# Optimization experiments

Measured on AMD Instinct MI355X. Metric: run time of the kernel, lower is better.

Reference implementation:

```python
import jax, jax.numpy as jnp
import numpy as np

DIM = 768
NUM_HEADS = 12
HEAD_DIM = DIM // NUM_HEADS
SCALE = HEAD_DIM ** -0.5
EPS = 1e-6


def setup_inputs() -> dict:
    key = jax.random.key(0)
    k_x, k_p, k_qkv, k_proj = jax.random.split(key, 4)
    B, N = 16, 577
    x = jax.random.normal(k_x, (B, N, DIM), dtype=jnp.float32)
    # binary keep/drop policy per token (as produced by an upstream gumbel gate)
    policy = jax.random.randint(k_p, (B, N, 1), 0, 2).astype(jnp.float32)
    Wqkv = jax.random.normal(k_qkv, (DIM, 3 * DIM), dtype=jnp.float32) * 0.02
    bqkv = jnp.zeros((3 * DIM,), dtype=jnp.float32)
    Wproj = jax.random.normal(k_proj, (DIM, DIM), dtype=jnp.float32) * 0.02
    bproj = jnp.zeros((DIM,), dtype=jnp.float32)
    return {"x": x, "policy": policy, "Wqkv": Wqkv, "bqkv": bqkv,
            "Wproj": Wproj, "bproj": bproj}


def reference(x, policy, Wqkv, bqkv, Wproj, bproj):
    B, N, C = x.shape
    # qkv projection -> [3, B, H, N, Dh]
    qkv = (x @ Wqkv + bqkv).reshape(B, N, 3, NUM_HEADS, HEAD_DIM)
    qkv = jnp.transpose(qkv, (2, 0, 3, 1, 4))
    q, k, v = qkv[0], qkv[1], qkv[2]
    # scaled attention logits [B, H, N, N]
    attn = jnp.einsum("bhnd,bhmd->bhnm", q, k) * SCALE
    # policy-masked softmax (training-mode formula: eye keeps self-attention alive)
    ap = policy.reshape(B, 1, 1, N)
    eye = jnp.eye(N, dtype=ap.dtype).reshape(1, 1, N, N)
    ap = ap + (1.0 - ap) * eye
    max_att = jnp.max(attn, axis=-1, keepdims=True)
    e = jnp.exp(attn - max_att) * ap
    attn = (e + EPS / N) / (jnp.sum(e, axis=-1, keepdims=True) + EPS)
    # attend and project
    out = jnp.einsum("bhnm,bhmd->bhnd", attn, v)
    out = jnp.transpose(out, (0, 2, 1, 3)).reshape(B, N, C)
    return out @ Wproj + bproj
```

## Files before the change

### kernel.cpp

```cpp
#include <hip/hip_runtime.h>
#include <hip/hip_bf16.h>

#define QKVC   2304
#define NHEAD  12
#define NTOK   577
#define NBATCH 16
#define NROWS  (NBATCH * NTOK)
#define NPAD   640
#define SCALE  0.125f
#define EPSV   1e-6f

typedef __bf16  bf16x8 __attribute__((ext_vector_type(8)));
typedef float   f32x4  __attribute__((ext_vector_type(4)));

__device__ __forceinline__ unsigned short f2bf(float f) {
    union { float f; unsigned u; } v; v.f = f;
    unsigned r = v.u + 0x7FFFu + ((v.u >> 16) & 1u);
    return (unsigned short)(r >> 16);
}
__device__ __forceinline__ unsigned short f2bf_trunc(float f) {
    return (unsigned short)(__float_as_uint(f) >> 16);
}
__device__ __forceinline__ f32x4 mfma16(bf16x8 a, bf16x8 b, f32x4 c) {
    return __builtin_amdgcn_mfma_f32_16x16x32_bf16(a, b, c, 0, 0, 0);
}

#define GLDS16(g, l) __builtin_amdgcn_global_load_lds( \
    (const __attribute__((address_space(1))) unsigned int*)(g), \
    (__attribute__((address_space(3))) unsigned int*)(l), 16, 0, 0)

__device__ void transpose_tile(const float* __restrict__ src, unsigned short* __restrict__ dst,
                               int K, int N, int bx, int by, int t) {
    __shared__ unsigned short lt[64 * 72];
    int n0 = bx * 64, k0 = by * 64;
    int kk = t >> 4, nn = (t & 15) * 4;
    for (int i = 0; i < 4; i++) {
        int kr = kk + i * 16;
        float4 v = *(const float4*)&src[(size_t)(k0 + kr) * N + n0 + nn];
        lt[(nn + 0) * 72 + kr] = f2bf(v.x);
        lt[(nn + 1) * 72 + kr] = f2bf(v.y);
        lt[(nn + 2) * 72 + kr] = f2bf(v.z);
        lt[(nn + 3) * 72 + kr] = f2bf(v.w);
    }
    __syncthreads();
    int n = t >> 2, seg = (t & 3) * 16;
    uint4 a = *(uint4*)&lt[n * 72 + seg];
    uint4 b = *(uint4*)&lt[n * 72 + seg + 8];
    *(uint4*)&dst[(size_t)(n0 + n) * K + k0 + seg]     = a;
    *(uint4*)&dst[(size_t)(n0 + n) * K + k0 + seg + 8] = b;
}

#define NCONV (NROWS * 768 / 4 / 256)
__global__ void k_prep(const float* __restrict__ x, unsigned short* __restrict__ xb,
                       const float* __restrict__ Wqkv, unsigned short* __restrict__ wqkvt,
                       const float* __restrict__ Wproj, unsigned short* __restrict__ wprojt) {
    int id = blockIdx.x, t = threadIdx.x;
    if (id < NCONV) {
        int idx = id * 256 + t;
        float4 v = ((const float4*)x)[idx];
        ushort4 o;
        o.x = f2bf(v.x); o.y = f2bf(v.y); o.z = f2bf(v.z); o.w = f2bf(v.w);
        ((ushort4*)xb)[idx] = o;
    } else if (id < NCONV + 432) {
        int i2 = id - NCONV;
        transpose_tile(Wqkv, wqkvt, 768, QKVC, i2 % 36, i2 / 36, t);
    } else {
        int i2 = id - NCONV - 432;
        transpose_tile(Wproj, wprojt, 768, 768, i2 % 12, i2 / 12, t);
    }
}

template <bool F32OUT>
__global__ __launch_bounds__(256, 2)
void k_gemm(const unsigned short* __restrict__ A, const unsigned short* __restrict__ B,
            const float* __restrict__ bias, void* __restrict__ outp, int Ncols,
            unsigned short* __restrict__ vt) {
    __shared__ unsigned short SL[32768];
    int t = threadIdx.x;
    int lane = t & 63, wave = t >> 6, quad = lane >> 4, l15 = lane & 15;
    int wm = wave >> 1, wn = wave & 1;
    int nT = Ncols >> 7;
    int mLocal = blockIdx.x & 7;
    int rest = blockIdx.x >> 3;
    int n0 = (rest % nT) * 128;
    int m0 = ((rest / nT) * 8 + mLocal) * 128;

    const unsigned short* ga0 = A + (size_t)(m0 + wave * 32 + (lane >> 2)) * 768 + (lane & 3) * 8;
    const unsigned short* ga1 = ga0 + (size_t)16 * 768;
    const unsigned short* gb0 = B + (size_t)(n0 + wave * 32 + (lane >> 2)) * 768 + (lane & 3) * 8;
    const unsigned short* gb1 = gb0 + (size_t)16 * 768;
    unsigned lo = wave * 1024;

    f32x4 acc[4][4] = {};

    GLDS16(ga0,      &SL[lo]);              GLDS16(ga1,      &SL[lo + 512]);
    GLDS16(ga0 + 32, &SL[4096 + lo]);       GLDS16(ga1 + 32, &SL[4096 + lo + 512]);
    GLDS16(gb0,      &SL[16384 + lo]);      GLDS16(gb1,      &SL[16384 + lo + 512]);
    GLDS16(gb0 + 32, &SL[20480 + lo]);      GLDS16(gb1 + 32, &SL[20480 + lo + 512]);

    #pragma unroll 2
    for (int kt = 0; kt < 12; kt++) {
        unsigned ab = (kt & 1) * 8192;
        unsigned bb = 16384 + ab;
        asm volatile("s_waitcnt vmcnt(0)" ::: "memory");
        asm volatile("s_barrier" ::: "memory");
        if (kt < 11) {
            unsigned na = 8192 - ab, nb = 16384 + na;
            int ko = (kt + 1) * 64;
            GLDS16(ga0 + ko,      &SL[na + lo]);        GLDS16(ga1 + ko,      &SL[na + lo + 512]);
            GLDS16(ga0 + ko + 32, &SL[na + 4096 + lo]); GLDS16(ga1 + ko + 32, &SL[na + 4096 + lo + 512]);
            GLDS16(gb0 + ko,      &SL[nb + lo]);        GLDS16(gb1 + ko,      &SL[nb + lo + 512]);
            GLDS16(gb0 + ko + 32, &SL[nb + 4096 + lo]); GLDS16(gb1 + ko + 32, &SL[nb + 4096 + lo + 512]);
        }
        for (int h = 0; h < 2; h++) {
            bf16x8 af[4], bfr[4];
            for (int i = 0; i < 4; i++) {
                af[i]  = *(const bf16x8*)&SL[ab + h * 4096 + (wm * 64 + i * 16 + l15) * 32 + quad * 8];
                bfr[i] = *(const bf16x8*)&SL[bb + h * 4096 + (wn * 64 + i * 16 + l15) * 32 + quad * 8];
            }
            for (int mi = 0; mi < 4; mi++)
                for (int ni = 0; ni < 4; ni++)
                    acc[mi][ni] = mfma16(af[mi], bfr[ni], acc[mi][ni]);
        }
    }
    asm volatile("" ::: "memory");

    if constexpr (F32OUT) {
        for (int ni = 0; ni < 4; ni++) {
            int col = n0 + wn * 64 + ni * 16 + l15;
            float bv = bias[col];
            for (int mi = 0; mi < 4; mi++) {
                int rowm = m0 + wm * 64 + mi * 16 + quad * 4;
                for (int r = 0; r < 4; r++) {
                    int m = rowm + r;
                    if (m < NROWS)
                        ((float*)outp)[(size_t)m * Ncols + col] = acc[mi][ni][r] + bv;
                }
            }
        }
    } else {
        __syncthreads();
        for (int ni = 0; ni < 4; ni++) {
            int colL = wn * 64 + ni * 16 + l15;
            float bv = bias[n0 + colL];
            for (int mi = 0; mi < 4; mi++) {
                int rowL = wm * 64 + mi * 16 + quad * 4;
                for (int r = 0; r < 4; r++)
                    SL[(rowL + r) * 132 + colL] = f2bf(acc[mi][ni][r] + bv);
            }
        }
        __syncthreads();
        if (n0 < 1536) {
            for (int rr = 0; rr < 8; rr++) {
                int row = rr * 16 + (t >> 4);
                int m = m0 + row;
                if (m < NROWS) {
                    uint4 v = *(uint4*)&SL[row * 132 + (t & 15) * 8];
                    *(uint4*)&((unsigned short*)outp)[(size_t)m * Ncols + n0 + (t & 15) * 8] = v;
                }
            }
        } else {
            int h0 = (n0 - 1536) >> 6;
            for (int i = 0; i < 32; i++) {
                int c = wave * 32 + i;
                int h = h0 + (c >> 6), d = c & 63;
                for (int half = 0; half < 2; half++) {
                    int lr = half * 64 + lane;
                    int m = m0 + lr;
                    if (m < NROWS) {
                        unsigned bbx = (unsigned)m / 577u;
                        int tok = m - (int)bbx * 577;
                        vt[(((size_t)bbx * NHEAD + h) * 64 + d) * NPAD + tok] =
                            SL[lr * 132 + c];
                    }
                }
            }
        }
    }
}

__global__ __launch_bounds__(256, 4)
void k_attn(const unsigned short* __restrict__ qkv, const unsigned short* __restrict__ vt,
            const float* __restrict__ policy, unsigned short* __restrict__ ao) {
    __shared__ unsigned short Ks[64 * 72];
    __shared__ unsigned short Vs[64 * 72];
    __shared__ unsigned short Ps[4][32 * 72];
    __shared__ float pol[NPAD];
    int t = threadIdx.x;
    int lane = t & 63, wave = t >> 6, quad = lane >> 4, l15 = lane & 15;
    int b = blockIdx.z, h = blockIdx.y, qt = blockIdx.x;
    const unsigned short* qbase = qkv + (size_t)(b * NTOK) * QKVC + h * 64;
    const unsigned short* kbase = qkv + (size_t)(b * NTOK) * QKVC + 768 + h * 64;
    const unsigned short* vbase = vt + (size_t)(b * NHEAD + h) * 64 * NPAD;

    for (int i = t; i < NPAD; i += 256)
        pol[i] = (i < NTOK) ? policy[b * NTOK + i] : 0.f;

    bf16x8 qf[2][2];
    for (int mi = 0; mi < 2; mi++) {
        const unsigned short* qp =
            qbase + (size_t)(qt * 128 + mi * 64 + wave * 16 + l15) * QKVC + quad * 8;
        qf[mi][0] = *(const bf16x8*)qp;
        qf[mi][1] = *(const bf16x8*)(qp + 32);
    }
    bf16x8 onesf;
    for (int j = 0; j < 8; j++) onesf[j] = (__bf16)1.0f;
    f32x4 o[2][4] = {};
    f32x4 ls[2] = {};
    int rowtok0[2];
    for (int mi = 0; mi < 2; mi++)
        rowtok0[mi] = qt * 128 + mi * 64 + wave * 16 + quad * 4;
    __syncthreads();

    for (int kt = 0; kt < 10; kt++) {
        int key0 = kt * 64;
        for (int i = t; i < 512; i += 256) {
            int row = i >> 3, seg = (i & 7) * 8;
            *(uint4*)&Ks[row * 72 + seg] = *(const uint4*)&kbase[(size_t)(key0 + row) * QKVC + seg];
            *(uint4*)&Vs[row * 72 + seg] = *(const uint4*)&vbase[(size_t)row * NPAD + key0 + seg];
        }
        __syncthreads();

        for (int ci = 0; ci < 4; ci++) {
            bf16x8 kf0 = *(const bf16x8*)&Ks[(ci * 16 + l15) * 72 + quad * 8];
            bf16x8 kf1 = *(const bf16x8*)&Ks[(ci * 16 + l15) * 72 + 32 + quad * 8];
            int col = key0 + ci * 16 + l15;
            float pc = pol[col];
            for (int mi = 0; mi < 2; mi++) {
                f32x4 a = {};
                a = mfma16(qf[mi][0], kf0, a);
                a = mfma16(qf[mi][1], kf1, a);
                for (int r = 0; r < 4; r++) {
                    float ap = (col == rowtok0[mi] + r) ? 1.f : pc;
                    float e = __expf(a[r] * SCALE) * ap;
                    Ps[wave][(mi * 16 + quad * 4 + r) * 72 + ci * 16 + l15] = f2bf_trunc(e);
                }
            }
        }
        __asm__ volatile("s_waitcnt lgkmcnt(0)" ::: "memory");
        bf16x8 pf[2][2];
        for (int mi = 0; mi < 2; mi++) {
            pf[mi][0] = *(const bf16x8*)&Ps[wave][(mi * 16 + l15) * 72 + quad * 8];
            pf[mi][1] = *(const bf16x8*)&Ps[wave][(mi * 16 + l15) * 72 + 32 + quad * 8];
            ls[mi] = mfma16(pf[mi][0], onesf, ls[mi]);
            ls[mi] = mfma16(pf[mi][1], onesf, ls[mi]);
        }
        for (int di = 0; di < 4; di++) {
            bf16x8 vf0 = *(const bf16x8*)&Vs[(di * 16 + l15) * 72 + quad * 8];
            bf16x8 vf1 = *(const bf16x8*)&Vs[(di * 16 + l15) * 72 + 32 + quad * 8];
            for (int mi = 0; mi < 2; mi++) {
                o[mi][di] = mfma16(pf[mi][0], vf0, o[mi][di]);
                o[mi][di] = mfma16(pf[mi][1], vf1, o[mi][di]);
            }
        }
        __syncthreads();
    }

    for (int mi = 0; mi < 2; mi++) {
        for (int r = 0; r < 4; r++) {
            int tok = rowtok0[mi] + r;
            if (tok < NTOK) {
                float inv = __builtin_amdgcn_rcpf(ls[mi][r] + EPSV);
                for (int di = 0; di < 4; di++) {
                    float val = o[mi][di][r] * inv;
                    ao[((size_t)(b * NTOK + tok)) * 768 + h * 64 + di * 16 + l15] = f2bf(val);
                }
            }
        }
    }
}

extern "C" void kernel_launch(void* const* d_in, const int* in_sizes, int n_in,
                              void* d_out, int out_size, void* d_ws, size_t ws_size,
                              hipStream_t stream) {
    const float* x      = (const float*)d_in[0];
    const float* policy = (const float*)d_in[1];
    const float* Wqkv   = (const float*)d_in[2];
    const float* bqkv   = (const float*)d_in[3];
    const float* Wproj  = (const float*)d_in[4];
    const float* bproj  = (const float*)d_in[5];
    float* out = (float*)d_out;

    unsigned short* p = (unsigned short*)d_ws;
    unsigned short* xb     = p;
    unsigned short* ao     = p; p += (size_t)NROWS * 768;
    unsigned short* wqkvt  = p; p += (size_t)QKVC * 768;
    unsigned short* wprojt = p; p += (size_t)768 * 768;
    unsigned short* qkvb   = p; p += (size_t)NROWS * QKVC;
    unsigned short* vt     = p; p += (size_t)NBATCH * NHEAD * 64 * NPAD;

    int mT = (NROWS + 127) / 128;
    int mG = (mT + 7) / 8;

    k_prep<<<NCONV + 432 + 144, 256, 0, stream>>>(x, xb, Wqkv, wqkvt, Wproj, wprojt);
    k_gemm<false><<<mG * 8 * (QKVC / 128), 256, 0, stream>>>(
        xb, wqkvt, bqkv, (void*)qkvb, QKVC, vt);
    k_attn<<<dim3(NPAD / 128, NHEAD, NBATCH), 256, 0, stream>>>(qkvb, vt, policy, ao);
    k_gemm<true><<<mG * 8 * (768 / 128), 256, 0, stream>>>(
        ao, wprojt, bproj, (void*)out, 768, nullptr);
}
```

Baseline: 203.3 us.

## Restructure GEMM to 256x128 tiles, 8 waves, 4-stage swizzled LDS pipeline

Rewrites the bf16 GEMM kernel to use 512-thread blocks computing 256x128 output tiles, with a 4-deep ring of 32-wide K slices loaded via global-to-LDS and partial vmcnt waits. It adds an XOR swizzle on LDS segments to reduce bank conflicts, s_setprio around the MFMA bursts, and an XCD-aware block remapping so that neighbouring tiles share an L2. The goal is deeper latency hiding and better operand reuse per block. In exchange it uses more LDS (96KB) and more accumulator registers per wave, and it pads the epilogue stride differently.

```diff
diff --git a/kernel.cpp b/kernel.cpp
--- a/kernel.cpp
+++ b/kernel.cpp
@@ -71,66 +71,84 @@
 }
 
 template <bool F32OUT>
-__global__ __launch_bounds__(256, 2)
+__global__ __launch_bounds__(512, 2)
 void k_gemm(const unsigned short* __restrict__ A, const unsigned short* __restrict__ B,
             const float* __restrict__ bias, void* __restrict__ outp, int Ncols,
             unsigned short* __restrict__ vt) {
-    __shared__ unsigned short SL[32768];
+    __shared__ unsigned short SL[49152];
     int t = threadIdx.x;
     int lane = t & 63, wave = t >> 6, quad = lane >> 4, l15 = lane & 15;
-    int wm = wave >> 1, wn = wave & 1;
+    int wm = wave >> 2, wn = wave & 3;
     int nT = Ncols >> 7;
-    int mLocal = blockIdx.x & 7;
-    int rest = blockIdx.x >> 3;
-    int n0 = (rest % nT) * 128;
-    int m0 = ((rest / nT) * 8 + mLocal) * 128;
-
-    const unsigned short* ga0 = A + (size_t)(m0 + wave * 32 + (lane >> 2)) * 768 + (lane & 3) * 8;
-    const unsigned short* ga1 = ga0 + (size_t)16 * 768;
-    const unsigned short* gb0 = B + (size_t)(n0 + wave * 32 + (lane >> 2)) * 768 + (lane & 3) * 8;
-    const unsigned short* gb1 = gb0 + (size_t)16 * 768;
-    unsigned lo = wave * 1024;
-
-    f32x4 acc[4][4] = {};
-
-    GLDS16(ga0,      &SL[lo]);              GLDS16(ga1,      &SL[lo + 512]);
-    GLDS16(ga0 + 32, &SL[4096 + lo]);       GLDS16(ga1 + 32, &SL[4096 + lo + 512]);
-    GLDS16(gb0,      &SL[16384 + lo]);      GLDS16(gb1,      &SL[16384 + lo + 512]);
-    GLDS16(gb0 + 32, &SL[20480 + lo]);      GLDS16(gb1 + 32, &SL[20480 + lo + 512]);
-
-    #pragma unroll 2
-    for (int kt = 0; kt < 12; kt++) {
-        unsigned ab = (kt & 1) * 8192;
-        unsigned bb = 16384 + ab;
-        asm volatile("s_waitcnt vmcnt(0)" ::: "memory");
+    int nwg = gridDim.x;
+
+    int q8 = nwg >> 3, r8 = nwg & 7;
+    int xcd = blockIdx.x & 7, idx = blockIdx.x >> 3;
+    int wg = (xcd < r8 ? xcd * (q8 + 1) : r8 * (q8 + 1) + (xcd - r8) * q8) + idx;
+    int m0 = (wg / nT) * 256;
+    int n0 = (wg % nT) * 128;
+
+    int srow = lane >> 2;
+    int sseg = (lane & 3) ^ ((lane >> 3) & 3);
+    const unsigned short* gA0 = A + (size_t)(m0 +       wave * 16 + srow) * 768 + sseg * 8;
+    const unsigned short* gA1 = A + (size_t)(m0 + 128 + wave * 16 + srow) * 768 + sseg * 8;
+    const unsigned short* gB0 = B + (size_t)(n0 +       wave * 16 + srow) * 768 + sseg * 8;
+
+    f32x4 acc[8][2] = {};
+
+    auto STAGE = [&](int sx) {
+        unsigned sa = (unsigned)(sx & 3) * 8192u + (unsigned)wave * 512u;
+        unsigned sb = 32768u + (unsigned)(sx & 3) * 4096u + (unsigned)wave * 512u;
+        int ko = sx * 32;
+        GLDS16(gA0 + ko, &SL[sa]);
+        GLDS16(gA1 + ko, &SL[sa + 4096]);
+        GLDS16(gB0 + ko, &SL[sb]);
+    };
+
+    auto STEP = [&](int s, bool stage) {
+        unsigned ab = (unsigned)(s & 3) * 8192u;
+        unsigned bb = 32768u + (unsigned)(s & 3) * 4096u;
+        unsigned ro = (unsigned)(quad ^ ((l15 >> 1) & 3)) * 8u;
+        bf16x8 af[8], bfr[2];
+        #pragma unroll
+        for (int i = 0; i < 8; i++)
+            af[i]  = *(const bf16x8*)&SL[ab + (unsigned)(wm * 128 + i * 16 + l15) * 32u + ro];
+        #pragma unroll
+        for (int i = 0; i < 2; i++)
+            bfr[i] = *(const bf16x8*)&SL[bb + (unsigned)(wn * 32 + i * 16 + l15) * 32u + ro];
+        if (stage) STAGE(s + 3);
+        asm volatile("s_waitcnt lgkmcnt(0)" ::: "memory");
+        __builtin_amdgcn_s_setprio(1);
+        #pragma unroll
+        for (int mi = 0; mi < 8; mi++)
+            #pragma unroll
+            for (int ni = 0; ni < 2; ni++)
+                acc[mi][ni] = mfma16(af[mi], bfr[ni], acc[mi][ni]);
+        __builtin_amdgcn_s_setprio(0);
+    };
+
+    STAGE(0); STAGE(1); STAGE(2);
+    for (int s = 0; s < 21; s++) {
+        asm volatile("s_waitcnt vmcnt(6)" ::: "memory");
         asm volatile("s_barrier" ::: "memory");
-        if (kt < 11) {
-            unsigned na = 8192 - ab, nb = 16384 + na;
-            int ko = (kt + 1) * 64;
-            GLDS16(ga0 + ko,      &SL[na + lo]);        GLDS16(ga1 + ko,      &SL[na + lo + 512]);
-            GLDS16(ga0 + ko + 32, &SL[na + 4096 + lo]); GLDS16(ga1 + ko + 32, &SL[na + 4096 + lo + 512]);
-            GLDS16(gb0 + ko,      &SL[nb + lo]);        GLDS16(gb1 + ko,      &SL[nb + lo + 512]);
-            GLDS16(gb0 + ko + 32, &SL[nb + 4096 + lo]); GLDS16(gb1 + ko + 32, &SL[nb + 4096 + lo + 512]);
-        }
-        for (int h = 0; h < 2; h++) {
-            bf16x8 af[4], bfr[4];
-            for (int i = 0; i < 4; i++) {
-                af[i]  = *(const bf16x8*)&SL[ab + h * 4096 + (wm * 64 + i * 16 + l15) * 32 + quad * 8];
-                bfr[i] = *(const bf16x8*)&SL[bb + h * 4096 + (wn * 64 + i * 16 + l15) * 32 + quad * 8];
-            }
-            for (int mi = 0; mi < 4; mi++)
-                for (int ni = 0; ni < 4; ni++)
-                    acc[mi][ni] = mfma16(af[mi], bfr[ni], acc[mi][ni]);
-        }
-    }
-    asm volatile("" ::: "memory");
+        STEP(s, true);
+    }
+    asm volatile("s_waitcnt vmcnt(6)" ::: "memory");
+    asm volatile("s_barrier" ::: "memory");
+    STEP(21, false);
+    asm volatile("s_waitcnt vmcnt(3)" ::: "memory");
+    asm volatile("s_barrier" ::: "memory");
+    STEP(22, false);
+    asm volatile("s_waitcnt vmcnt(0)" ::: "memory");
+    asm volatile("s_barrier" ::: "memory");
+    STEP(23, false);
 
     if constexpr (F32OUT) {
-        for (int ni = 0; ni < 4; ni++) {
-            int col = n0 + wn * 64 + ni * 16 + l15;
+        for (int ni = 0; ni < 2; ni++) {
+            int col = n0 + wn * 32 + ni * 16 + l15;
             float bv = bias[col];
-            for (int mi = 0; mi < 4; mi++) {
-                int rowm = m0 + wm * 64 + mi * 16 + quad * 4;
+            for (int mi = 0; mi < 8; mi++) {
+                int rowm = m0 + wm * 128 + mi * 16 + quad * 4;
                 for (int r = 0; r < 4; r++) {
                     int m = rowm + r;
                     if (m < NROWS)
@@ -140,38 +158,38 @@
         }
     } else {
         __syncthreads();
-        for (int ni = 0; ni < 4; ni++) {
-            int colL = wn * 64 + ni * 16 + l15;
+        for (int ni = 0; ni < 2; ni++) {
+            int colL = wn * 32 + ni * 16 + l15;
             float bv = bias[n0 + colL];
-            for (int mi = 0; mi < 4; mi++) {
-                int rowL = wm * 64 + mi * 16 + quad * 4;
+            for (int mi = 0; mi < 8; mi++) {
+                int rowL = wm * 128 + mi * 16 + quad * 4;
                 for (int r = 0; r < 4; r++)
-                    SL[(rowL + r) * 132 + colL] = f2bf(acc[mi][ni][r] + bv);
+                    SL[(rowL + r) * 136 + colL] = f2bf(acc[mi][ni][r] + bv);
             }
         }
         __syncthreads();
         if (n0 < 1536) {
             for (int rr = 0; rr < 8; rr++) {
-                int row = rr * 16 + (t >> 4);
+                int row = rr * 32 + (t >> 4);
                 int m = m0 + row;
                 if (m < NROWS) {
-                    uint4 v = *(uint4*)&SL[row * 132 + (t & 15) * 8];
+                    uint4 v = *(uint4*)&SL[row * 136 + (t & 15) * 8];
                     *(uint4*)&((unsigned short*)outp)[(size_t)m * Ncols + n0 + (t & 15) * 8] = v;
                 }
             }
         } else {
             int h0 = (n0 - 1536) >> 6;
-            for (int i = 0; i < 32; i++) {
-                int c = wave * 32 + i;
+            for (int i = 0; i < 16; i++) {
+                int c = wave * 16 + i;
                 int h = h0 + (c >> 6), d = c & 63;
-                for (int half = 0; half < 2; half++) {
+                for (int half = 0; half < 4; half++) {
                     int lr = half * 64 + lane;
                     int m = m0 + lr;
                     if (m < NROWS) {
                         unsigned bbx = (unsigned)m / 577u;
                         int tok = m - (int)bbx * 577;
                         vt[(((size_t)bbx * NHEAD + h) * 64 + d) * NPAD + tok] =
-                            SL[lr * 132 + c];
+                            SL[lr * 136 + c];
                     }
                 }
             }
@@ -289,13 +307,12 @@
     unsigned short* qkvb   = p; p += (size_t)NROWS * QKVC;
     unsigned short* vt     = p; p += (size_t)NBATCH * NHEAD * 64 * NPAD;
 
-    int mT = (NROWS + 127) / 128;
-    int mG = (mT + 7) / 8;
+    int mT = (NROWS + 255) / 256;
 
     k_prep<<<NCONV + 432 + 144, 256, 0, stream>>>(x, xb, Wqkv, wqkvt, Wproj, wprojt);
-    k_gemm<false><<<mG * 8 * (QKVC / 128), 256, 0, stream>>>(
+    k_gemm<false><<<mT * (QKVC / 128), 512, 0, stream>>>(
         xb, wqkvt, bqkv, (void*)qkvb, QKVC, vt);
     k_attn<<<dim3(NPAD / 128, NHEAD, NBATCH), 256, 0, stream>>>(qkvb, vt, policy, ao);
-    k_gemm<true><<<mG * 8 * (768 / 128), 256, 0, stream>>>(
+    k_gemm<true><<<mT * (768 / 128), 512, 0, stream>>>(
         ao, wprojt, bproj, (void*)out, 768, nullptr);
 }
```

Result: no change. 206.7 us (+1.7%).
